# Performance work log

Hardware: AMD Instinct MI355X
Metric: run time of the kernel (lower is better)

Reference implementation:

```python
import jax, jax.numpy as jnp
import numpy as np

B, N, D, E = 4, 100000, 128, 262144
HID, OUT, EXTRA = 128, 128, 1


def setup_inputs() -> dict:
    key = jax.random.key(0)
    k1, k2, k3, k4, k5 = jax.random.split(key, 5)
    node_emb = jax.random.normal(k1, (B, N, D), dtype=jnp.float32)
    edge_index = jax.random.randint(k2, (B, E, 2), 0, N, dtype=jnp.int64)
    edge_sel = jax.random.uniform(k3, (B, E, EXTRA), dtype=jnp.float32)
    W1 = jax.random.normal(k4, (2 * D + EXTRA, HID), dtype=jnp.float32) * (1.0 / np.sqrt(2 * D + EXTRA))
    b1 = jnp.zeros((HID,), dtype=jnp.float32)
    W2 = jax.random.normal(k5, (HID, OUT), dtype=jnp.float32) * (1.0 / np.sqrt(HID))
    b2 = jnp.zeros((OUT,), dtype=jnp.float32)
    return {"node_emb": node_emb, "edge_index": edge_index, "edge_sel": edge_sel,
            "W1": W1, "b1": b1, "W2": W2, "b2": b2}


def reference(node_emb, edge_index, edge_sel, W1, b1, W2, b2):
    n = node_emb.shape[1]
    idx_u = jnp.clip(edge_index[..., 0], 0, n - 1)  # [B,E]
    idx_v = jnp.clip(edge_index[..., 1], 0, n - 1)  # [B,E]
    batch = jnp.arange(node_emb.shape[0])[:, None]  # [B,1]
    u = node_emb[batch, idx_u]  # [B,E,D]
    v = node_emb[batch, idx_v]  # [B,E,D]
    x = jnp.concatenate([u, v, edge_sel.astype(jnp.float32)], axis=-1)  # [B,E,2D+1]
    h = jax.nn.relu(jnp.einsum('bef,fh->beh', x, W1) + b1)
    return jax.nn.relu(jnp.einsum('beh,ho->beo', h, W2) + b2)
```

## Files before the change

kernel.cpp:

```cpp
#include <hip/hip_runtime.h>
#include <stdint.h>

#define BB 4
#define NN 100000
#define DD 128
#define EE 262144
#define HH 128
#define OO 128

typedef __attribute__((ext_vector_type(4))) float f32x4;
typedef __attribute__((ext_vector_type(8))) __bf16 bf16x8;
typedef __attribute__((ext_vector_type(8))) unsigned short u16x8;

static __device__ __forceinline__ unsigned short f2bf(float f) {
    union { float f; unsigned u; } v; v.f = f;
    return (unsigned short)((v.u + 0x7fffu + ((v.u >> 16) & 1u)) >> 16);
}

__global__ __launch_bounds__(256) void prep_w1(const float* __restrict__ W1,
                                               unsigned short* __restrict__ w1f) {
    int t = blockIdx.x * 256 + threadIdx.x;
    int k = t >> 7, n = t & 127;
    int f = ((((k >> 5) * 8 + (n >> 4)) * 64) + ((k >> 3) & 3) * 16 + (n & 15)) * 8 + (k & 7);
    w1f[f] = f2bf(W1[t]);
}

__global__ __launch_bounds__(256) void prep_w2(const float* __restrict__ W2,
                                               unsigned short* __restrict__ w2f) {
    int t = blockIdx.x * 256 + threadIdx.x;
    int k = t >> 7, n = t & 127;
    int f = ((((k >> 5) * 8 + (n >> 4)) * 64) + ((k >> 3) & 3) * 16 + (n & 15)) * 8 + (k & 7);
    w2f[f] = f2bf(W2[t]);
}

__global__ __launch_bounds__(256) void prep_node(const float* __restrict__ ne,
                                                 unsigned short* __restrict__ nb) {
    size_t t = (size_t)blockIdx.x * 256 + threadIdx.x;
    const f32x4* s = (const f32x4*)ne + (t << 1);
    f32x4 a = s[0], b = s[1];
    u16x8 o;
    o[0] = f2bf(a[0]); o[1] = f2bf(a[1]); o[2] = f2bf(a[2]); o[3] = f2bf(a[3]);
    o[4] = f2bf(b[0]); o[5] = f2bf(b[1]); o[6] = f2bf(b[2]); o[7] = f2bf(b[3]);
    *((u16x8*)nb + t) = o;
}

template<bool BF16N, bool W2LDS>
__global__ __launch_bounds__(256, 4) void edge_mlp(
    const float* __restrict__ node_emb,
    const unsigned short* __restrict__ node_bf,
    const int* __restrict__ edge_index,
    const float* __restrict__ edge_sel,
    const float* __restrict__ W1,
    const float* __restrict__ b1,
    const float* __restrict__ W2,
    const float* __restrict__ b2,
    const unsigned short* __restrict__ w1f,
    const unsigned short* __restrict__ w2f,
    float* __restrict__ out)
{
    __shared__ unsigned short hst[4][2][16 * 136];
    __shared__ unsigned short w2s[W2LDS ? 16384 : 1];

    const int tid = threadIdx.x;

    if constexpr (W2LDS) {
        for (int s = tid; s < 16384; s += 256) {
            int k = s >> 7, n = s & 127;
            int f = ((((k >> 5) * 8 + (n >> 4)) * 64) + ((k >> 3) & 3) * 16 + (n & 15)) * 8 + (k & 7);
            w2s[f] = f2bf(W2[s]);
        }
        __syncthreads();
    }

    const int lane = tid & 63;
    const int wv = tid >> 6;
    const int nl = lane & 15;
    const int quad = lane >> 4;

    float b1v[8], w1cv[8];
#pragma unroll
    for (int nt = 0; nt < 8; ++nt) {
        b1v[nt] = b1[nt * 16 + nl];
        w1cv[nt] = W1[256 * 128 + nt * 16 + nl];
    }

    const int eb = blockIdx.x * 128 + wv * 32;
    const int bat = eb >> 18;
    const unsigned nbase = (unsigned)bat * (NN * DD);

    unsigned ou[2], ov[2];
#pragma unroll
    for (int mt = 0; mt < 2; ++mt) {
        int e = eb + mt * 16 + nl;
        int iu = edge_index[(size_t)e * 2 + 0];
        int iv = edge_index[(size_t)e * 2 + 1];
        iu = min(max(iu, 0), NN - 1);
        iv = min(max(iv, 0), NN - 1);
        ou[mt] = nbase + (unsigned)iu * DD + quad * 8;
        ov[mt] = nbase + (unsigned)iv * DD + quad * 8;
    }

    f32x4 acc[2][8];
#pragma unroll
    for (int mt = 0; mt < 2; ++mt)
#pragma unroll
        for (int nt = 0; nt < 8; ++nt)
            acc[mt][nt] = f32x4{0.f, 0.f, 0.f, 0.f};

    const bf16x8* w1b = (const bf16x8*)w1f;
#pragma unroll
    for (int kt = 0; kt < 8; ++kt) {
        bf16x8 af[2];
#pragma unroll
        for (int mt = 0; mt < 2; ++mt) {
            unsigned o = ((kt < 4) ? ou[mt] : ov[mt]) + (kt & 3) * 32;
            if constexpr (BF16N) {
                af[mt] = *(const bf16x8*)(node_bf + o);
            } else {
                f32x4 x0 = *(const f32x4*)(node_emb + o);
                f32x4 x1 = *(const f32x4*)(node_emb + o + 4);
                bf16x8 a;
                a[0] = (__bf16)x0[0]; a[1] = (__bf16)x0[1];
                a[2] = (__bf16)x0[2]; a[3] = (__bf16)x0[3];
                a[4] = (__bf16)x1[0]; a[5] = (__bf16)x1[1];
                a[6] = (__bf16)x1[2]; a[7] = (__bf16)x1[3];
                af[mt] = a;
            }
        }
#pragma unroll
        for (int nt = 0; nt < 8; ++nt) {
            bf16x8 bf = w1b[(kt * 8 + nt) * 64 + lane];
            acc[0][nt] = __builtin_amdgcn_mfma_f32_16x16x32_bf16(af[0], bf, acc[0][nt], 0, 0, 0);
            acc[1][nt] = __builtin_amdgcn_mfma_f32_16x16x32_bf16(af[1], bf, acc[1][nt], 0, 0, 0);
        }
    }

#pragma unroll
    for (int q = 0; q < 2; ++q) {
        float sel[4];
#pragma unroll
        for (int i = 0; i < 4; ++i)
            sel[i] = edge_sel[(size_t)(eb + q * 16 + quad * 4 + i)];
        unsigned short* hw = hst[wv][q];
#pragma unroll
        for (int nt = 0; nt < 8; ++nt) {
#pragma unroll
            for (int i = 0; i < 4; ++i) {
                float hv = acc[q][nt][i] + sel[i] * w1cv[nt] + b1v[nt];
                hv = fmaxf(hv, 0.f);
                hw[(quad * 4 + i) * 136 + nt * 16 + nl] = f2bf(hv);
            }
        }
    }

    bf16x8 ha[2][4];
#pragma unroll
    for (int q = 0; q < 2; ++q)
#pragma unroll
        for (int kt2 = 0; kt2 < 4; ++kt2)
            ha[q][kt2] = *(const bf16x8*)(hst[wv][q] + nl * 136 + kt2 * 32 + quad * 8);

    f32x4 a2[2][8];
#pragma unroll
    for (int q = 0; q < 2; ++q)
#pragma unroll
        for (int nt = 0; nt < 8; ++nt)
            a2[q][nt] = f32x4{0.f, 0.f, 0.f, 0.f};

    const bf16x8* w2b = (const bf16x8*)(W2LDS ? (const unsigned short*)w2s : w2f);
#pragma unroll
    for (int kt2 = 0; kt2 < 4; ++kt2) {
#pragma unroll
        for (int nt = 0; nt < 8; ++nt) {
            bf16x8 bf = w2b[(kt2 * 8 + nt) * 64 + lane];
            a2[0][nt] = __builtin_amdgcn_mfma_f32_16x16x32_bf16(ha[0][kt2], bf, a2[0][nt], 0, 0, 0);
            a2[1][nt] = __builtin_amdgcn_mfma_f32_16x16x32_bf16(ha[1][kt2], bf, a2[1][nt], 0, 0, 0);
        }
    }

    float b2v[8];
#pragma unroll
    for (int nt = 0; nt < 8; ++nt)
        b2v[nt] = b2[nt * 16 + nl];

#pragma unroll
    for (int q = 0; q < 2; ++q) {
#pragma unroll
        for (int nt = 0; nt < 8; ++nt) {
#pragma unroll
            for (int i = 0; i < 4; ++i) {
                float o = a2[q][nt][i] + b2v[nt];
                o = fmaxf(o, 0.f);
                __builtin_nontemporal_store(
                    o, &out[(size_t)(eb + q * 16 + quad * 4 + i) * OO + nt * 16 + nl]);
            }
        }
    }
}

extern "C" void kernel_launch(void* const* d_in, const int* in_sizes, int n_in,
                              void* d_out, int out_size, void* d_ws, size_t ws_size,
                              hipStream_t stream) {
    const float* node_emb  = (const float*)d_in[0];
    const int*   edge_index= (const int*)d_in[1];
    const float* edge_sel  = (const float*)d_in[2];
    const float* W1        = (const float*)d_in[3];
    const float* b1        = (const float*)d_in[4];
    const float* W2        = (const float*)d_in[5];
    const float* b2        = (const float*)d_in[6];
    float* out             = (float*)d_out;

    unsigned short* w1f = (unsigned short*)d_ws;
    const size_t NODE_BYTES = (size_t)BB * NN * DD * 2;
    const size_t NEED_B = 65536 + 32768;
    const size_t NEED_A = NEED_B + NODE_BYTES;

    prep_w1<<<dim3(128), dim3(256), 0, stream>>>(W1, w1f);

    if (ws_size >= NEED_A) {
        unsigned short* w2f = w1f + 32768;
        unsigned short* nbf = w2f + 16384;
        prep_w2<<<dim3(64), dim3(256), 0, stream>>>(W2, w2f);
        prep_node<<<dim3(25000), dim3(256), 0, stream>>>(node_emb, nbf);
        edge_mlp<true, false><<<dim3(8192), dim3(256), 0, stream>>>(
            node_emb, nbf, edge_index, edge_sel, W1, b1, W2, b2, w1f, w2f, out);
    } else if (ws_size >= NEED_B) {
        unsigned short* w2f = w1f + 32768;
        prep_w2<<<dim3(64), dim3(256), 0, stream>>>(W2, w2f);
        edge_mlp<false, false><<<dim3(8192), dim3(256), 0, stream>>>(
            node_emb, nullptr, edge_index, edge_sel, W1, b1, W2, b2, w1f, w2f, out);
    } else {
        edge_mlp<false, true><<<dim3(8192), dim3(256), 0, stream>>>(
            node_emb, nullptr, edge_index, edge_sel, W1, b1, W2, b2, w1f, nullptr, out);
    }
}
```

Before: 940.2 us.

## Process four edge tiles per wave with double-buffered gather prefetch

Each wave now handles four 32-edge tiles in a loop instead of one, and the grid shrinks accordingly. In the bf16 path, the node gather for the next tile is issued before the current tile's epilogue and layer-2 MFMAs, so gather latency can overlap compute. W2 rows are permuted so the hidden activations can be written to LDS as packed 8-element vectors instead of scalar stores. Edge indices and edge_sel are loaded as vectors. The double buffer raises register pressure, so the occupancy hint drops from 4 to 3 (or 2) blocks, and the nontemporal output stores become ordinary stores.

```diff
diff --git a/kernel.cpp b/kernel.cpp
--- a/kernel.cpp
+++ b/kernel.cpp
@@ -29,7 +29,8 @@
                                                unsigned short* __restrict__ w2f) {
     int t = blockIdx.x * 256 + threadIdx.x;
     int k = t >> 7, n = t & 127;
-    int f = ((((k >> 5) * 8 + (n >> 4)) * 64) + ((k >> 3) & 3) * 16 + (n & 15)) * 8 + (k & 7);
+    int k2 = (k & 15) * 8 + (k >> 4);
+    int f = ((((k2 >> 5) * 8 + (n >> 4)) * 64) + ((k2 >> 3) & 3) * 16 + (n & 15)) * 8 + (k2 & 7);
     w2f[f] = f2bf(W2[t]);
 }
 
@@ -44,8 +45,100 @@
     *((u16x8*)nb + t) = o;
 }
 
+
+static __device__ __forceinline__ void gather_tile(
+    const unsigned short* __restrict__ nb, const int* __restrict__ ei,
+    int e0t, unsigned nbase, int nl, int quad, bf16x8* dst)
+{
+    unsigned ou[2], ov[2];
+#pragma unroll
+    for (int mt = 0; mt < 2; ++mt) {
+        int e = e0t + mt * 16 + nl;
+        int2 p = ((const int2*)ei)[e];
+        int iu = min(max(p.x, 0), NN - 1);
+        int iv = min(max(p.y, 0), NN - 1);
+        ou[mt] = nbase + (unsigned)iu * DD + quad * 8;
+        ov[mt] = nbase + (unsigned)iv * DD + quad * 8;
+    }
+#pragma unroll
+    for (int kt = 0; kt < 8; ++kt)
+#pragma unroll
+        for (int mt = 0; mt < 2; ++mt)
+            dst[kt * 2 + mt] = *(const bf16x8*)(nb + ((kt < 4) ? ou[mt] : ov[mt]) + (kt & 3) * 32);
+}
+
+static __device__ __forceinline__ void layer1(
+    const bf16x8* af, const bf16x8* __restrict__ w1b, int lane, f32x4 acc[2][8])
+{
+#pragma unroll
+    for (int mt = 0; mt < 2; ++mt)
+#pragma unroll
+        for (int nt = 0; nt < 8; ++nt)
+            acc[mt][nt] = f32x4{0.f, 0.f, 0.f, 0.f};
+#pragma unroll
+    for (int kt = 0; kt < 8; ++kt) {
+#pragma unroll
+        for (int nt = 0; nt < 8; ++nt) {
+            bf16x8 bf = w1b[(kt * 8 + nt) * 64 + lane];
+            acc[0][nt] = __builtin_amdgcn_mfma_f32_16x16x32_bf16(af[kt * 2 + 0], bf, acc[0][nt], 0, 0, 0);
+            acc[1][nt] = __builtin_amdgcn_mfma_f32_16x16x32_bf16(af[kt * 2 + 1], bf, acc[1][nt], 0, 0, 0);
+        }
+    }
+}
+
+static __device__ __forceinline__ void finish_tile(
+    f32x4 acc[2][8], const f32x4* sel, int eb,
+    const float* b1v, const float* w1cv, const float* b2v,
+    unsigned short* hw,
+    const bf16x8* __restrict__ w2b,
+    int lane, int nl, int quad, float* __restrict__ out)
+{
+#pragma unroll
+    for (int q = 0; q < 2; ++q) {
+#pragma unroll
+        for (int i = 0; i < 4; ++i) {
+            bf16x8 hv;
+#pragma unroll
+            for (int nt = 0; nt < 8; ++nt) {
+                float h = acc[q][nt][i] + sel[q][i] * w1cv[nt] + b1v[nt];
+                hv[nt] = (__bf16)fmaxf(h, 0.f);
+            }
+            *(bf16x8*)(hw + q * (16 * 136) + (quad * 4 + i) * 136 + nl * 8) = hv;
+        }
+    }
+
+    f32x4 a2[2][8];
+#pragma unroll
+    for (int q = 0; q < 2; ++q)
+#pragma unroll
+        for (int nt = 0; nt < 8; ++nt)
+            a2[q][nt] = f32x4{0.f, 0.f, 0.f, 0.f};
+
+#pragma unroll
+    for (int kt2 = 0; kt2 < 4; ++kt2) {
+        bf16x8 h0 = *(const bf16x8*)(hw + nl * 136 + kt2 * 32 + quad * 8);
+        bf16x8 h1 = *(const bf16x8*)(hw + 16 * 136 + nl * 136 + kt2 * 32 + quad * 8);
+#pragma unroll
+        for (int nt = 0; nt < 8; ++nt) {
+            bf16x8 bf = w2b[(kt2 * 8 + nt) * 64 + lane];
+            a2[0][nt] = __builtin_amdgcn_mfma_f32_16x16x32_bf16(h0, bf, a2[0][nt], 0, 0, 0);
+            a2[1][nt] = __builtin_amdgcn_mfma_f32_16x16x32_bf16(h1, bf, a2[1][nt], 0, 0, 0);
+        }
+    }
+
+#pragma unroll
+    for (int q = 0; q < 2; ++q)
+#pragma unroll
+        for (int nt = 0; nt < 8; ++nt)
+#pragma unroll
+            for (int i = 0; i < 4; ++i) {
+                float o = a2[q][nt][i] + b2v[nt];
+                out[(size_t)(eb + q * 16 + quad * 4 + i) * OO + nt * 16 + nl] = fmaxf(o, 0.f);
+            }
+}
+
 template<bool BF16N, bool W2LDS>
-__global__ __launch_bounds__(256, 4) void edge_mlp(
+__global__ __launch_bounds__(256, BF16N ? 3 : 2) void edge_mlp(
     const float* __restrict__ node_emb,
     const unsigned short* __restrict__ node_bf,
     const int* __restrict__ edge_index,
@@ -66,7 +159,8 @@
     if constexpr (W2LDS) {
         for (int s = tid; s < 16384; s += 256) {
             int k = s >> 7, n = s & 127;
-            int f = ((((k >> 5) * 8 + (n >> 4)) * 64) + ((k >> 3) & 3) * 16 + (n & 15)) * 8 + (k & 7);
+            int k2 = (k & 15) * 8 + (k >> 4);
+            int f = ((((k2 >> 5) * 8 + (n >> 4)) * 64) + ((k2 >> 3) & 3) * 16 + (n & 15)) * 8 + (k2 & 7);
             w2s[f] = f2bf(W2[s]);
         }
         __syncthreads();
@@ -77,123 +171,80 @@
     const int nl = lane & 15;
     const int quad = lane >> 4;
 
-    float b1v[8], w1cv[8];
+    float b1v[8], w1cv[8], b2v[8];
 #pragma unroll
     for (int nt = 0; nt < 8; ++nt) {
         b1v[nt] = b1[nt * 16 + nl];
         w1cv[nt] = W1[256 * 128 + nt * 16 + nl];
-    }
-
-    const int eb = blockIdx.x * 128 + wv * 32;
-    const int bat = eb >> 18;
-    const unsigned nbase = (unsigned)bat * (NN * DD);
-
-    unsigned ou[2], ov[2];
-#pragma unroll
-    for (int mt = 0; mt < 2; ++mt) {
-        int e = eb + mt * 16 + nl;
-        int iu = edge_index[(size_t)e * 2 + 0];
-        int iv = edge_index[(size_t)e * 2 + 1];
-        iu = min(max(iu, 0), NN - 1);
-        iv = min(max(iv, 0), NN - 1);
-        ou[mt] = nbase + (unsigned)iu * DD + quad * 8;
-        ov[mt] = nbase + (unsigned)iv * DD + quad * 8;
-    }
-
-    f32x4 acc[2][8];
-#pragma unroll
-    for (int mt = 0; mt < 2; ++mt)
-#pragma unroll
-        for (int nt = 0; nt < 8; ++nt)
-            acc[mt][nt] = f32x4{0.f, 0.f, 0.f, 0.f};
+        b2v[nt] = b2[nt * 16 + nl];
+    }
+
+    const int e0 = (blockIdx.x * 4 + wv) * 128;
+    const unsigned nbase = (unsigned)(e0 >> 18) * (NN * DD);
 
     const bf16x8* w1b = (const bf16x8*)w1f;
-#pragma unroll
-    for (int kt = 0; kt < 8; ++kt) {
-        bf16x8 af[2];
-#pragma unroll
-        for (int mt = 0; mt < 2; ++mt) {
-            unsigned o = ((kt < 4) ? ou[mt] : ov[mt]) + (kt & 3) * 32;
-            if constexpr (BF16N) {
-                af[mt] = *(const bf16x8*)(node_bf + o);
-            } else {
-                f32x4 x0 = *(const f32x4*)(node_emb + o);
-                f32x4 x1 = *(const f32x4*)(node_emb + o + 4);
-                bf16x8 a;
-                a[0] = (__bf16)x0[0]; a[1] = (__bf16)x0[1];
-                a[2] = (__bf16)x0[2]; a[3] = (__bf16)x0[3];
-                a[4] = (__bf16)x1[0]; a[5] = (__bf16)x1[1];
-                a[6] = (__bf16)x1[2]; a[7] = (__bf16)x1[3];
-                af[mt] = a;
-            }
-        }
-#pragma unroll
-        for (int nt = 0; nt < 8; ++nt) {
-            bf16x8 bf = w1b[(kt * 8 + nt) * 64 + lane];
-            acc[0][nt] = __builtin_amdgcn_mfma_f32_16x16x32_bf16(af[0], bf, acc[0][nt], 0, 0, 0);
-            acc[1][nt] = __builtin_amdgcn_mfma_f32_16x16x32_bf16(af[1], bf, acc[1][nt], 0, 0, 0);
-        }
-    }
-
-#pragma unroll
-    for (int q = 0; q < 2; ++q) {
-        float sel[4];
-#pragma unroll
-        for (int i = 0; i < 4; ++i)
-            sel[i] = edge_sel[(size_t)(eb + q * 16 + quad * 4 + i)];
-        unsigned short* hw = hst[wv][q];
-#pragma unroll
-        for (int nt = 0; nt < 8; ++nt) {
-#pragma unroll
-            for (int i = 0; i < 4; ++i) {
-                float hv = acc[q][nt][i] + sel[i] * w1cv[nt] + b1v[nt];
-                hv = fmaxf(hv, 0.f);
-                hw[(quad * 4 + i) * 136 + nt * 16 + nl] = f2bf(hv);
-            }
-        }
-    }
-
-    bf16x8 ha[2][4];
-#pragma unroll
-    for (int q = 0; q < 2; ++q)
-#pragma unroll
-        for (int kt2 = 0; kt2 < 4; ++kt2)
-            ha[q][kt2] = *(const bf16x8*)(hst[wv][q] + nl * 136 + kt2 * 32 + quad * 8);
-
-    f32x4 a2[2][8];
-#pragma unroll
-    for (int q = 0; q < 2; ++q)
-#pragma unroll
-        for (int nt = 0; nt < 8; ++nt)
-            a2[q][nt] = f32x4{0.f, 0.f, 0.f, 0.f};
-
     const bf16x8* w2b = (const bf16x8*)(W2LDS ? (const unsigned short*)w2s : w2f);
-#pragma unroll
-    for (int kt2 = 0; kt2 < 4; ++kt2) {
-#pragma unroll
-        for (int nt = 0; nt < 8; ++nt) {
-            bf16x8 bf = w2b[(kt2 * 8 + nt) * 64 + lane];
-            a2[0][nt] = __builtin_amdgcn_mfma_f32_16x16x32_bf16(ha[0][kt2], bf, a2[0][nt], 0, 0, 0);
-            a2[1][nt] = __builtin_amdgcn_mfma_f32_16x16x32_bf16(ha[1][kt2], bf, a2[1][nt], 0, 0, 0);
-        }
-    }
-
-    float b2v[8];
-#pragma unroll
-    for (int nt = 0; nt < 8; ++nt)
-        b2v[nt] = b2[nt * 16 + nl];
-
-#pragma unroll
-    for (int q = 0; q < 2; ++q) {
-#pragma unroll
-        for (int nt = 0; nt < 8; ++nt) {
-#pragma unroll
-            for (int i = 0; i < 4; ++i) {
-                float o = a2[q][nt][i] + b2v[nt];
-                o = fmaxf(o, 0.f);
-                __builtin_nontemporal_store(
-                    o, &out[(size_t)(eb + q * 16 + quad * 4 + i) * OO + nt * 16 + nl]);
-            }
+    unsigned short* hw = &hst[wv][0][0];
+
+    if constexpr (BF16N) {
+        bf16x8 afbuf[2][16];
+        f32x4 selbuf[2][2];
+
+        gather_tile(node_bf, edge_index, e0, nbase, nl, quad, afbuf[0]);
+        selbuf[0][0] = *(const f32x4*)(edge_sel + e0 + quad * 4);
+        selbuf[0][1] = *(const f32x4*)(edge_sel + e0 + 16 + quad * 4);
+
+#pragma unroll
+        for (int t = 0; t < 4; ++t) {
+            const int eb = e0 + t * 32;
+            f32x4 acc[2][8];
+            layer1(afbuf[t & 1], w1b, lane, acc);
+
+            if (t < 3) {
+                gather_tile(node_bf, edge_index, eb + 32, nbase, nl, quad, afbuf[(t + 1) & 1]);
+                selbuf[(t + 1) & 1][0] = *(const f32x4*)(edge_sel + eb + 32 + quad * 4);
+                selbuf[(t + 1) & 1][1] = *(const f32x4*)(edge_sel + eb + 48 + quad * 4);
+            }
+
+            finish_tile(acc, selbuf[t & 1], eb, b1v, w1cv, b2v, hw, w2b,
+                        lane, nl, quad, out);
+        }
+    } else {
+#pragma unroll
+        for (int t = 0; t < 4; ++t) {
+            const int eb = e0 + t * 32;
+            unsigned ou[2], ov[2];
+#pragma unroll
+            for (int mt = 0; mt < 2; ++mt) {
+                int e = eb + mt * 16 + nl;
+                int2 p = ((const int2*)edge_index)[e];
+                int iu = min(max(p.x, 0), NN - 1);
+                int iv = min(max(p.y, 0), NN - 1);
+                ou[mt] = nbase + (unsigned)iu * DD + quad * 8;
+                ov[mt] = nbase + (unsigned)iv * DD + quad * 8;
+            }
+            bf16x8 af[16];
+#pragma unroll
+            for (int kt = 0; kt < 8; ++kt)
+#pragma unroll
+                for (int mt = 0; mt < 2; ++mt) {
+                    unsigned o = ((kt < 4) ? ou[mt] : ov[mt]) + (kt & 3) * 32;
+                    f32x4 x0 = *(const f32x4*)(node_emb + o);
+                    f32x4 x1 = *(const f32x4*)(node_emb + o + 4);
+                    bf16x8 a;
+                    a[0] = (__bf16)x0[0]; a[1] = (__bf16)x0[1];
+                    a[2] = (__bf16)x0[2]; a[3] = (__bf16)x0[3];
+                    a[4] = (__bf16)x1[0]; a[5] = (__bf16)x1[1];
+                    a[6] = (__bf16)x1[2]; a[7] = (__bf16)x1[3];
+                    af[kt * 2 + mt] = a;
+                }
+            f32x4 sel[2];
+            sel[0] = *(const f32x4*)(edge_sel + eb + quad * 4);
+            sel[1] = *(const f32x4*)(edge_sel + eb + 16 + quad * 4);
+
+            f32x4 acc[2][8];
+            layer1(af, w1b, lane, acc);
+            finish_tile(acc, sel, eb, b1v, w1cv, b2v, hw, w2b, lane, nl, quad, out);
         }
     }
 }
@@ -222,15 +273,15 @@
         unsigned short* nbf = w2f + 16384;
         prep_w2<<<dim3(64), dim3(256), 0, stream>>>(W2, w2f);
         prep_node<<<dim3(25000), dim3(256), 0, stream>>>(node_emb, nbf);
-        edge_mlp<true, false><<<dim3(8192), dim3(256), 0, stream>>>(
+        edge_mlp<true, false><<<dim3(2048), dim3(256), 0, stream>>>(
             node_emb, nbf, edge_index, edge_sel, W1, b1, W2, b2, w1f, w2f, out);
     } else if (ws_size >= NEED_B) {
         unsigned short* w2f = w1f + 32768;
         prep_w2<<<dim3(64), dim3(256), 0, stream>>>(W2, w2f);
-        edge_mlp<false, false><<<dim3(8192), dim3(256), 0, stream>>>(
+        edge_mlp<false, false><<<dim3(2048), dim3(256), 0, stream>>>(
             node_emb, nullptr, edge_index, edge_sel, W1, b1, W2, b2, w1f, w2f, out);
     } else {
-        edge_mlp<false, true><<<dim3(8192), dim3(256), 0, stream>>>(
+        edge_mlp<false, true><<<dim3(2048), dim3(256), 0, stream>>>(
             node_emb, nullptr, edge_index, edge_sel, W1, b1, W2, b2, w1f, nullptr, out);
     }
 }
```

Result: slower. 2.425 ms (+157.9%).

## Stage edge-MLP output through LDS for wide stores and permute W2 rows

Applied to the files above, without the earlier changes.

The final ReLU output tile is staged in per-wave LDS and written to global memory as 16-byte vectors covering whole rows, replacing scattered scalar nontemporal stores. W2's K rows are permuted in the prep kernels so the hidden activations can be written to LDS as packed bf16x8 vectors instead of scalar shorts. Biases now initialise the MFMA accumulators, and edge_index and edge_sel are read with vector loads. The launch-bounds occupancy hint drops from 4 to 3 blocks per CU, giving more registers at the cost of fewer waves to hide gather latency. Dropping the nontemporal hint may increase cache pollution from the large output stream.

```diff
diff --git a/kernel.cpp b/kernel.cpp
--- a/kernel.cpp
+++ b/kernel.cpp
@@ -29,7 +29,8 @@
                                                unsigned short* __restrict__ w2f) {
     int t = blockIdx.x * 256 + threadIdx.x;
     int k = t >> 7, n = t & 127;
-    int f = ((((k >> 5) * 8 + (n >> 4)) * 64) + ((k >> 3) & 3) * 16 + (n & 15)) * 8 + (k & 7);
+    int k2 = (k & 15) * 8 + (k >> 4);
+    int f = ((((k2 >> 5) * 8 + (n >> 4)) * 64) + ((k2 >> 3) & 3) * 16 + (n & 15)) * 8 + (k2 & 7);
     w2f[f] = f2bf(W2[t]);
 }
 
@@ -45,7 +46,7 @@
 }
 
 template<bool BF16N, bool W2LDS>
-__global__ __launch_bounds__(256, 4) void edge_mlp(
+__global__ __launch_bounds__(256, 3) void edge_mlp(
     const float* __restrict__ node_emb,
     const unsigned short* __restrict__ node_bf,
     const int* __restrict__ edge_index,
@@ -66,7 +67,8 @@
     if constexpr (W2LDS) {
         for (int s = tid; s < 16384; s += 256) {
             int k = s >> 7, n = s & 127;
-            int f = ((((k >> 5) * 8 + (n >> 4)) * 64) + ((k >> 3) & 3) * 16 + (n & 15)) * 8 + (k & 7);
+            int k2 = (k & 15) * 8 + (k >> 4);
+            int f = ((((k2 >> 5) * 8 + (n >> 4)) * 64) + ((k2 >> 3) & 3) * 16 + (n & 15)) * 8 + (k2 & 7);
             w2s[f] = f2bf(W2[s]);
         }
         __syncthreads();
@@ -77,46 +79,50 @@
     const int nl = lane & 15;
     const int quad = lane >> 4;
 
-    float b1v[8], w1cv[8];
+    float b1v[8], w1cv[8], b2v[8];
 #pragma unroll
     for (int nt = 0; nt < 8; ++nt) {
         b1v[nt] = b1[nt * 16 + nl];
         w1cv[nt] = W1[256 * 128 + nt * 16 + nl];
+        b2v[nt] = b2[nt * 16 + nl];
     }
 
     const int eb = blockIdx.x * 128 + wv * 32;
-    const int bat = eb >> 18;
-    const unsigned nbase = (unsigned)bat * (NN * DD);
+    const unsigned nbase = (unsigned)(eb >> 18) * (NN * DD);
 
     unsigned ou[2], ov[2];
 #pragma unroll
     for (int mt = 0; mt < 2; ++mt) {
         int e = eb + mt * 16 + nl;
-        int iu = edge_index[(size_t)e * 2 + 0];
-        int iv = edge_index[(size_t)e * 2 + 1];
-        iu = min(max(iu, 0), NN - 1);
-        iv = min(max(iv, 0), NN - 1);
+        int2 p = ((const int2*)edge_index)[e];
+        int iu = min(max(p.x, 0), NN - 1);
+        int iv = min(max(p.y, 0), NN - 1);
         ou[mt] = nbase + (unsigned)iu * DD + quad * 8;
         ov[mt] = nbase + (unsigned)iv * DD + quad * 8;
     }
 
+    f32x4 sel[2];
+    sel[0] = *(const f32x4*)(edge_sel + eb + quad * 4);
+    sel[1] = *(const f32x4*)(edge_sel + eb + 16 + quad * 4);
+
     f32x4 acc[2][8];
 #pragma unroll
     for (int mt = 0; mt < 2; ++mt)
 #pragma unroll
         for (int nt = 0; nt < 8; ++nt)
-            acc[mt][nt] = f32x4{0.f, 0.f, 0.f, 0.f};
+            acc[mt][nt] = f32x4{b1v[nt], b1v[nt], b1v[nt], b1v[nt]};
 
     const bf16x8* w1b = (const bf16x8*)w1f;
 #pragma unroll
     for (int kt = 0; kt < 8; ++kt) {
-        bf16x8 af[2];
-#pragma unroll
-        for (int mt = 0; mt < 2; ++mt) {
-            unsigned o = ((kt < 4) ? ou[mt] : ov[mt]) + (kt & 3) * 32;
-            if constexpr (BF16N) {
-                af[mt] = *(const bf16x8*)(node_bf + o);
-            } else {
+        bf16x8 af0, af1;
+        if constexpr (BF16N) {
+            af0 = *(const bf16x8*)(node_bf + ((kt < 4) ? ou[0] : ov[0]) + (kt & 3) * 32);
+            af1 = *(const bf16x8*)(node_bf + ((kt < 4) ? ou[1] : ov[1]) + (kt & 3) * 32);
+        } else {
+#pragma unroll
+            for (int mt = 0; mt < 2; ++mt) {
+                unsigned o = ((kt < 4) ? ou[mt] : ov[mt]) + (kt & 3) * 32;
                 f32x4 x0 = *(const f32x4*)(node_emb + o);
                 f32x4 x1 = *(const f32x4*)(node_emb + o + 4);
                 bf16x8 a;
@@ -124,76 +130,66 @@
                 a[2] = (__bf16)x0[2]; a[3] = (__bf16)x0[3];
                 a[4] = (__bf16)x1[0]; a[5] = (__bf16)x1[1];
                 a[6] = (__bf16)x1[2]; a[7] = (__bf16)x1[3];
-                af[mt] = a;
+                if (mt == 0) af0 = a; else af1 = a;
             }
         }
 #pragma unroll
         for (int nt = 0; nt < 8; ++nt) {
             bf16x8 bf = w1b[(kt * 8 + nt) * 64 + lane];
-            acc[0][nt] = __builtin_amdgcn_mfma_f32_16x16x32_bf16(af[0], bf, acc[0][nt], 0, 0, 0);
-            acc[1][nt] = __builtin_amdgcn_mfma_f32_16x16x32_bf16(af[1], bf, acc[1][nt], 0, 0, 0);
-        }
-    }
-
+            acc[0][nt] = __builtin_amdgcn_mfma_f32_16x16x32_bf16(af0, bf, acc[0][nt], 0, 0, 0);
+            acc[1][nt] = __builtin_amdgcn_mfma_f32_16x16x32_bf16(af1, bf, acc[1][nt], 0, 0, 0);
+        }
+    }
+
+    unsigned short* hw = &hst[wv][0][0];
 #pragma unroll
     for (int q = 0; q < 2; ++q) {
-        float sel[4];
-#pragma unroll
-        for (int i = 0; i < 4; ++i)
-            sel[i] = edge_sel[(size_t)(eb + q * 16 + quad * 4 + i)];
-        unsigned short* hw = hst[wv][q];
-#pragma unroll
-        for (int nt = 0; nt < 8; ++nt) {
-#pragma unroll
-            for (int i = 0; i < 4; ++i) {
-                float hv = acc[q][nt][i] + sel[i] * w1cv[nt] + b1v[nt];
-                hv = fmaxf(hv, 0.f);
-                hw[(quad * 4 + i) * 136 + nt * 16 + nl] = f2bf(hv);
+#pragma unroll
+        for (int i = 0; i < 4; ++i) {
+            bf16x8 hv;
+#pragma unroll
+            for (int nt = 0; nt < 8; ++nt) {
+                float h = fmaf(sel[q][i], w1cv[nt], acc[q][nt][i]);
+                hv[nt] = (__bf16)fmaxf(h, 0.f);
             }
-        }
-    }
-
-    bf16x8 ha[2][4];
+            *(bf16x8*)(hw + q * (16 * 136) + (quad * 4 + i) * 136 + nl * 8) = hv;
+        }
+    }
+
+    f32x4 a2[2][8];
 #pragma unroll
     for (int q = 0; q < 2; ++q)
 #pragma unroll
-        for (int kt2 = 0; kt2 < 4; ++kt2)
-            ha[q][kt2] = *(const bf16x8*)(hst[wv][q] + nl * 136 + kt2 * 32 + quad * 8);
-
-    f32x4 a2[2][8];
-#pragma unroll
-    for (int q = 0; q < 2; ++q)
-#pragma unroll
         for (int nt = 0; nt < 8; ++nt)
-            a2[q][nt] = f32x4{0.f, 0.f, 0.f, 0.f};
+            a2[q][nt] = f32x4{b2v[nt], b2v[nt], b2v[nt], b2v[nt]};
 
     const bf16x8* w2b = (const bf16x8*)(W2LDS ? (const unsigned short*)w2s : w2f);
 #pragma unroll
     for (int kt2 = 0; kt2 < 4; ++kt2) {
+        bf16x8 h0 = *(const bf16x8*)(hw + nl * 136 + kt2 * 32 + quad * 8);
+        bf16x8 h1 = *(const bf16x8*)(hw + 16 * 136 + nl * 136 + kt2 * 32 + quad * 8);
 #pragma unroll
         for (int nt = 0; nt < 8; ++nt) {
             bf16x8 bf = w2b[(kt2 * 8 + nt) * 64 + lane];
-            a2[0][nt] = __builtin_amdgcn_mfma_f32_16x16x32_bf16(ha[0][kt2], bf, a2[0][nt], 0, 0, 0);
-            a2[1][nt] = __builtin_amdgcn_mfma_f32_16x16x32_bf16(ha[1][kt2], bf, a2[1][nt], 0, 0, 0);
-        }
-    }
-
-    float b2v[8];
-#pragma unroll
-    for (int nt = 0; nt < 8; ++nt)
-        b2v[nt] = b2[nt * 16 + nl];
-
+            a2[0][nt] = __builtin_amdgcn_mfma_f32_16x16x32_bf16(h0, bf, a2[0][nt], 0, 0, 0);
+            a2[1][nt] = __builtin_amdgcn_mfma_f32_16x16x32_bf16(h1, bf, a2[1][nt], 0, 0, 0);
+        }
+    }
+
+    float* fb = (float*)hw;
+    const int rl = lane >> 5;
+    const int cl = lane & 31;
 #pragma unroll
     for (int q = 0; q < 2; ++q) {
 #pragma unroll
-        for (int nt = 0; nt < 8; ++nt) {
-#pragma unroll
-            for (int i = 0; i < 4; ++i) {
-                float o = a2[q][nt][i] + b2v[nt];
-                o = fmaxf(o, 0.f);
-                __builtin_nontemporal_store(
-                    o, &out[(size_t)(eb + q * 16 + quad * 4 + i) * OO + nt * 16 + nl]);
-            }
+        for (int nt = 0; nt < 8; ++nt)
+#pragma unroll
+            for (int i = 0; i < 4; ++i)
+                fb[(quad * 4 + i) * 132 + nt * 16 + nl] = fmaxf(a2[q][nt][i], 0.f);
+#pragma unroll
+        for (int r = 0; r < 8; ++r) {
+            f32x4 v = *(const f32x4*)(fb + (2 * r + rl) * 132 + cl * 4);
+            *(f32x4*)(out + (size_t)(eb + q * 16 + 2 * r + rl) * OO + cl * 4) = v;
         }
     }
 }
```

New measurement: 925.0 us. No clear change (-1.6%).
